# Kernel optimization log

Measured on AMD Instinct MI355X. Metric: run time of the kernel, lower is better.

## Reference

```python
import jax, jax.numpy as jnp
import numpy as np

N_NODES = 50000
N_EDGES = 600000
IN_FEATS = 128
OUT_FEATS = 128


def setup_inputs() -> dict:
    key = jax.random.key(0)
    k1, k2, k3, k4, k5 = jax.random.split(key, 5)
    feature = jax.random.normal(k1, (N_NODES, IN_FEATS), dtype=jnp.float32)
    src = jax.random.randint(k2, (N_EDGES,), 0, N_NODES, dtype=jnp.int64)
    dst = jax.random.randint(k3, (N_EDGES,), 0, N_NODES, dtype=jnp.int64)
    # nn.Linear params (PyTorch stores weight as [out, in])
    bound = 1.0 / np.sqrt(IN_FEATS)
    W = jax.random.uniform(k4, (OUT_FEATS, IN_FEATS), dtype=jnp.float32, minval=-bound, maxval=bound)
    b = jax.random.uniform(k5, (OUT_FEATS,), dtype=jnp.float32, minval=-bound, maxval=bound)
    return {"feature": feature, "W": W, "b": b, "src": src, "dst": dst}


def reference(feature, W, b, src, dst):
    # copy_src + sum: aggregate src features onto dst nodes (SpMM)
    agg = jax.ops.segment_sum(feature[src], dst, num_segments=N_NODES)  # [N, in]
    # linear + tanh
    return jnp.tanh(agg @ W.T + b)  # [N, out]
```

## Files before the change

kernel.cpp:

```cpp
#include <hip/hip_runtime.h>
#include <hip/hip_fp16.h>
#include <math.h>

constexpr int kNodes = 50000;
constexpr int kEdges = 600000;
constexpr int kF     = 128;
constexpr int kNPB   = 64;
constexpr int kCap   = 48;

constexpr int kGemmB = (kNodes + kNPB - 1) / kNPB;
constexpr int kFillB = (kEdges + 255) / 256;

constexpr size_t kOffWt     = 0;
constexpr size_t kOffCursor = 65536;
constexpr size_t kOffBucket = 65536 + 200192;
constexpr size_t kOffGpk    = kOffBucket + (size_t)kNodes * kCap * 4;
constexpr size_t kWsNeeded  = kOffGpk + (size_t)kNodes * kF * 2;

static __device__ __forceinline__ unsigned int packh2(float a, float b) {
    __half2 h = __floats2half2_rn(a, b);
    return *reinterpret_cast<unsigned int*>(&h);
}

__global__ __launch_bounds__(256) void prep0(const float* __restrict__ W,
                                             float* __restrict__ Wt,
                                             int* __restrict__ cursor) {
    int gid = blockIdx.x * 256 + threadIdx.x;
    if (gid < kF * kF) {
        int k = gid >> 7;
        int o = gid & (kF - 1);
        Wt[gid] = W[o * kF + k];
    }
    if (gid < kNodes) cursor[gid] = 0;
}

__global__ __launch_bounds__(256, 4) void gemm_fill(const float* __restrict__ F,
                                                    const float* __restrict__ Wt,
                                                    const int* __restrict__ src,
                                                    const int* __restrict__ dst,
                                                    int* __restrict__ cursor,
                                                    int* __restrict__ bucket,
                                                    uint2* __restrict__ Gpk2) {
    __shared__ float sF[kNPB * kF];

    const int t = threadIdx.x;

    if (blockIdx.x >= kGemmB) {
        int e = (blockIdx.x - kGemmB) * 256 + t;
        if (e < kEdges) {
            int d = dst[e];
            int p = atomicAdd(&cursor[d], 1);
            if (p < kCap) bucket[d * kCap + p] = src[e];
        }
        return;
    }

    const int n0 = blockIdx.x * kNPB;
    const int rows = min(kNPB, kNodes - n0);
    for (int i = t * 4; i < rows * kF; i += 256 * 4) {
        *reinterpret_cast<float4*>(&sF[i]) =
            *reinterpret_cast<const float4*>(F + (size_t)n0 * kF + i);
    }
    __syncthreads();

    const int tn = t >> 5;
    const int to = t & 31;
    const int nb = tn * 8;

    float acc[8][4];
#pragma unroll
    for (int n = 0; n < 8; ++n)
#pragma unroll
        for (int j = 0; j < 4; ++j) acc[n][j] = 0.0f;

    for (int k = 0; k < kF; k += 4) {
        float4 wt[4];
#pragma unroll
        for (int i = 0; i < 4; ++i)
            wt[i] = *reinterpret_cast<const float4*>(Wt + (k + i) * kF + to * 4);
#pragma unroll
        for (int n = 0; n < 8; ++n) {
            float4 av = *reinterpret_cast<const float4*>(&sF[(nb + n) * kF + k]);
#pragma unroll
            for (int j = 0; j < 4; ++j) {
                const float* wj0 = reinterpret_cast<const float*>(&wt[0]);
                const float* wj1 = reinterpret_cast<const float*>(&wt[1]);
                const float* wj2 = reinterpret_cast<const float*>(&wt[2]);
                const float* wj3 = reinterpret_cast<const float*>(&wt[3]);
                acc[n][j] += av.x * wj0[j];
                acc[n][j] += av.y * wj1[j];
                acc[n][j] += av.z * wj2[j];
                acc[n][j] += av.w * wj3[j];
            }
        }
    }

#pragma unroll
    for (int n = 0; n < 8; ++n) {
        int node = n0 + nb + n;
        if (node < kNodes) {
            uint2 p;
            p.x = packh2(acc[n][0], acc[n][1]);
            p.y = packh2(acc[n][2], acc[n][3]);
            Gpk2[(size_t)node * 32 + to] = p;
        }
    }
}

__global__ __launch_bounds__(256) void gather_tanh(const uint4* __restrict__ Gpk4,
                                                   const int* __restrict__ bucket,
                                                   const int* __restrict__ cursor,
                                                   const float* __restrict__ bias,
                                                   float* __restrict__ out) {
    const int wave = (blockIdx.x * 256 + threadIdx.x) >> 6;
    const int lane = threadIdx.x & 63;
    if (wave >= kNodes) return;
    const int grp = lane >> 4;
    const int sub = lane & 15;

    const int deg = min(cursor[wave], kCap);
    const int base = wave * kCap;

    int eid = (lane < deg) ? bucket[base + lane] : 0;

    float acc[8];
#pragma unroll
    for (int i = 0; i < 8; ++i) acc[i] = 0.0f;

    const int iters = (deg + 3) >> 2;
#pragma unroll 2
    for (int i = 0; i < iters; ++i) {
        const int j = grp + 4 * i;
        const bool valid = (j < deg);
        int s = __shfl(eid, valid ? j : 0);
        if (valid) {
            uint4 u = Gpk4[(size_t)s * 16 + sub];
            const __half2* hp = reinterpret_cast<const __half2*>(&u);
#pragma unroll
            for (int q = 0; q < 4; ++q) {
                float2 f = __half22float2(hp[q]);
                acc[2 * q]     += f.x;
                acc[2 * q + 1] += f.y;
            }
        }
    }

#pragma unroll
    for (int i = 0; i < 8; ++i) {
        acc[i] += __shfl_xor(acc[i], 16);
        acc[i] += __shfl_xor(acc[i], 32);
    }

    if (grp == 0) {
        float4 b0 = *reinterpret_cast<const float4*>(bias + sub * 8);
        float4 b1 = *reinterpret_cast<const float4*>(bias + sub * 8 + 4);
        float4 r0, r1;
        r0.x = 1.0f - 2.0f / (__expf(2.0f * (acc[0] + b0.x)) + 1.0f);
        r0.y = 1.0f - 2.0f / (__expf(2.0f * (acc[1] + b0.y)) + 1.0f);
        r0.z = 1.0f - 2.0f / (__expf(2.0f * (acc[2] + b0.z)) + 1.0f);
        r0.w = 1.0f - 2.0f / (__expf(2.0f * (acc[3] + b0.w)) + 1.0f);
        r1.x = 1.0f - 2.0f / (__expf(2.0f * (acc[4] + b1.x)) + 1.0f);
        r1.y = 1.0f - 2.0f / (__expf(2.0f * (acc[5] + b1.y)) + 1.0f);
        r1.z = 1.0f - 2.0f / (__expf(2.0f * (acc[6] + b1.z)) + 1.0f);
        r1.w = 1.0f - 2.0f / (__expf(2.0f * (acc[7] + b1.w)) + 1.0f);
        float4* dst = reinterpret_cast<float4*>(out + (size_t)wave * kF + sub * 8);
        dst[0] = r0;
        dst[1] = r1;
    }
}

__global__ __launch_bounds__(256) void scatter_add(const float* __restrict__ feature,
                                                   const int* __restrict__ src,
                                                   const int* __restrict__ dst,
                                                   float* __restrict__ agg) {
    int gid = blockIdx.x * 256 + threadIdx.x;
    int e = gid >> 5;
    int c = (gid & 31) << 2;
    float4 v = *reinterpret_cast<const float4*>(feature + (size_t)src[e] * kF + c);
    float* p = agg + (size_t)dst[e] * kF + c;
    atomicAdd(p + 0, v.x);
    atomicAdd(p + 1, v.y);
    atomicAdd(p + 2, v.z);
    atomicAdd(p + 3, v.w);
}

__global__ __launch_bounds__(256, 4) void linear_tanh(float* __restrict__ inout,
                                                      const float* __restrict__ Wt,
                                                      const float* __restrict__ bias) {
    __shared__ float sAgg[kNPB * kF];
    __shared__ float sB[kF];
    const int t  = threadIdx.x;
    const int n0 = blockIdx.x * kNPB;
    if (t < kF) sB[t] = bias[t];
    const int rows = min(kNPB, kNodes - n0);
    for (int i = t * 4; i < rows * kF; i += 256 * 4)
        *reinterpret_cast<float4*>(&sAgg[i]) =
            *reinterpret_cast<const float4*>(inout + (size_t)n0 * kF + i);
    __syncthreads();
    const int tn = t >> 5, to = t & 31, nb = tn * 8;
    float acc[8][4];
#pragma unroll
    for (int n = 0; n < 8; ++n)
#pragma unroll
        for (int j = 0; j < 4; ++j) acc[n][j] = 0.0f;
    for (int k = 0; k < kF; k += 4) {
        float4 wt[4];
#pragma unroll
        for (int i = 0; i < 4; ++i)
            wt[i] = *reinterpret_cast<const float4*>(Wt + (k + i) * kF + to * 4);
#pragma unroll
        for (int n = 0; n < 8; ++n) {
            float4 av = *reinterpret_cast<const float4*>(&sAgg[(nb + n) * kF + k]);
#pragma unroll
            for (int j = 0; j < 4; ++j) {
                const float* w0 = reinterpret_cast<const float*>(&wt[0]);
                const float* w1 = reinterpret_cast<const float*>(&wt[1]);
                const float* w2 = reinterpret_cast<const float*>(&wt[2]);
                const float* w3 = reinterpret_cast<const float*>(&wt[3]);
                acc[n][j] += av.x * w0[j] + av.y * w1[j] + av.z * w2[j] + av.w * w3[j];
            }
        }
    }
#pragma unroll
    for (int n = 0; n < 8; ++n) {
        int node = n0 + nb + n;
        if (node < kNodes) {
            float4 r;
            r.x = 1.0f - 2.0f / (__expf(2.0f * (acc[n][0] + sB[to * 4 + 0])) + 1.0f);
            r.y = 1.0f - 2.0f / (__expf(2.0f * (acc[n][1] + sB[to * 4 + 1])) + 1.0f);
            r.z = 1.0f - 2.0f / (__expf(2.0f * (acc[n][2] + sB[to * 4 + 2])) + 1.0f);
            r.w = 1.0f - 2.0f / (__expf(2.0f * (acc[n][3] + sB[to * 4 + 3])) + 1.0f);
            *reinterpret_cast<float4*>(inout + (size_t)node * kF + to * 4) = r;
        }
    }
}

extern "C" void kernel_launch(void* const* d_in, const int* in_sizes, int n_in,
                              void* d_out, int out_size, void* d_ws, size_t ws_size,
                              hipStream_t stream) {
    const float* feature = (const float*)d_in[0];
    const float* W       = (const float*)d_in[1];
    const float* b       = (const float*)d_in[2];
    const int*   src     = (const int*)d_in[3];
    const int*   dst     = (const int*)d_in[4];
    float* out = (float*)d_out;

    char* ws = (char*)d_ws;
    float* Wt     = (float*)(ws + kOffWt);
    int*   cursor = (int*)(ws + kOffCursor);
    int*   bucket = (int*)(ws + kOffBucket);
    uint2* Gpk2   = (uint2*)(ws + kOffGpk);

    if (ws_size >= kWsNeeded) {
        prep0<<<(kNodes + 255) / 256, 256, 0, stream>>>(W, Wt, cursor);
        gemm_fill<<<kGemmB + kFillB, 256, 0, stream>>>(
            feature, Wt, src, dst, cursor, bucket, Gpk2);
        gather_tanh<<<(kNodes + 3) / 4, 256, 0, stream>>>(
            (const uint4*)Gpk2, bucket, cursor, b, out);
    } else {
        prep0<<<(kNodes + 255) / 256, 256, 0, stream>>>(W, Wt, cursor);
        hipMemsetAsync(out, 0, (size_t)kNodes * kF * sizeof(float), stream);
        scatter_add<<<(kEdges * 32) / 256, 256, 0, stream>>>(feature, src, dst, out);
        linear_tanh<<<(kNodes + kNPB - 1) / kNPB, 256, 0, stream>>>(out, Wt, b);
    }
}
```

Before: 145.9 us.

## Use fp16 packed dot products in transform GEMM with LDS-staged weights

The per-node linear transform now converts features and W to half precision in shared memory and accumulates with packed fp16 dot2 instructions into fp32. Each thread now handles output columns strided by 32, so the gather kernel reads a permuted bias and writes outputs with strided float2 stores. The goal is to cut ALU and LDS traffic in the GEMM phase. In exchange, every block repacks the full weight matrix, LDS use grows so occupancy bound drops to 3, and rounding inputs to fp16 reduces accuracy.

Result: slower. 163.6 us (+12.2%).

```diff
diff --git a/kernel.cpp b/kernel.cpp
--- a/kernel.cpp
+++ b/kernel.cpp
@@ -15,7 +15,20 @@
 constexpr size_t kOffCursor = 65536;
 constexpr size_t kOffBucket = 65536 + 200192;
 constexpr size_t kOffGpk    = kOffBucket + (size_t)kNodes * kCap * 4;
-constexpr size_t kWsNeeded  = kOffGpk + (size_t)kNodes * kF * 2;
+constexpr size_t kOffBiasP  = kOffGpk + (size_t)kNodes * kF * 2;
+constexpr size_t kWsNeeded  = kOffBiasP + kF * 4;
+
+typedef _Float16 v2h __attribute__((ext_vector_type(2)));
+union H8 { uint4 u; v2h h[4]; };
+
+#if __has_builtin(__builtin_amdgcn_fdot2)
+#define FDOT2(a, b, c) __builtin_amdgcn_fdot2((a), (b), (c), false)
+#else
+static __device__ __forceinline__ float fdot2_emul(v2h a, v2h b, float c) {
+    return c + (float)a[0] * (float)b[0] + (float)a[1] * (float)b[1];
+}
+#define FDOT2(a, b, c) fdot2_emul((a), (b), (c))
+#endif
 
 static __device__ __forceinline__ unsigned int packh2(float a, float b) {
     __half2 h = __floats2half2_rn(a, b);
@@ -23,25 +36,29 @@
 }
 
 __global__ __launch_bounds__(256) void prep0(const float* __restrict__ W,
+                                             const float* __restrict__ b,
                                              float* __restrict__ Wt,
-                                             int* __restrict__ cursor) {
+                                             int* __restrict__ cursor,
+                                             float* __restrict__ bias_p) {
     int gid = blockIdx.x * 256 + threadIdx.x;
     if (gid < kF * kF) {
         int k = gid >> 7;
         int o = gid & (kF - 1);
         Wt[gid] = W[o * kF + k];
     }
+    if (gid < kF) bias_p[gid] = b[(gid >> 2) + 32 * (gid & 3)];
     if (gid < kNodes) cursor[gid] = 0;
 }
 
-__global__ __launch_bounds__(256, 4) void gemm_fill(const float* __restrict__ F,
-                                                    const float* __restrict__ Wt,
+__global__ __launch_bounds__(256, 3) void gemm_fill(const float* __restrict__ F,
+                                                    const float* __restrict__ Wg,
                                                     const int* __restrict__ src,
                                                     const int* __restrict__ dst,
                                                     int* __restrict__ cursor,
                                                     int* __restrict__ bucket,
                                                     uint2* __restrict__ Gpk2) {
-    __shared__ float sF[kNPB * kF];
+    __shared__ unsigned short sW[kF * kF];
+    __shared__ unsigned short sF[kNPB * kF];
 
     const int t = threadIdx.x;
 
@@ -57,9 +74,25 @@
 
     const int n0 = blockIdx.x * kNPB;
     const int rows = min(kNPB, kNodes - n0);
+
+    for (int idx = t; idx < kF * 16; idx += 256) {
+        int o  = idx >> 4;
+        int K8 = idx & 15;
+        const float4* wp = reinterpret_cast<const float4*>(Wg + o * kF + K8 * 8);
+        float4 w0 = wp[0], w1 = wp[1];
+        uint4 pk;
+        pk.x = packh2(w0.x, w0.y);
+        pk.y = packh2(w0.z, w0.w);
+        pk.z = packh2(w1.x, w1.y);
+        pk.w = packh2(w1.z, w1.w);
+        *reinterpret_cast<uint4*>(&sW[(K8 * kF + o) * 8]) = pk;
+    }
     for (int i = t * 4; i < rows * kF; i += 256 * 4) {
-        *reinterpret_cast<float4*>(&sF[i]) =
-            *reinterpret_cast<const float4*>(F + (size_t)n0 * kF + i);
+        float4 v = *reinterpret_cast<const float4*>(F + (size_t)n0 * kF + i);
+        uint2 pk;
+        pk.x = packh2(v.x, v.y);
+        pk.y = packh2(v.z, v.w);
+        *reinterpret_cast<uint2*>(&sF[i]) = pk;
     }
     __syncthreads();
 
@@ -73,24 +106,21 @@
 #pragma unroll
         for (int j = 0; j < 4; ++j) acc[n][j] = 0.0f;
 
-    for (int k = 0; k < kF; k += 4) {
-        float4 wt[4];
-#pragma unroll
-        for (int i = 0; i < 4; ++i)
-            wt[i] = *reinterpret_cast<const float4*>(Wt + (k + i) * kF + to * 4);
+#pragma unroll 4
+    for (int K8 = 0; K8 < 16; ++K8) {
+        H8 w[4];
+#pragma unroll
+        for (int j = 0; j < 4; ++j)
+            w[j].u = *reinterpret_cast<const uint4*>(&sW[(K8 * kF + to + 32 * j) * 8]);
 #pragma unroll
         for (int n = 0; n < 8; ++n) {
-            float4 av = *reinterpret_cast<const float4*>(&sF[(nb + n) * kF + k]);
+            H8 a;
+            a.u = *reinterpret_cast<const uint4*>(&sF[(nb + n) * kF + K8 * 8]);
 #pragma unroll
             for (int j = 0; j < 4; ++j) {
-                const float* wj0 = reinterpret_cast<const float*>(&wt[0]);
-                const float* wj1 = reinterpret_cast<const float*>(&wt[1]);
-                const float* wj2 = reinterpret_cast<const float*>(&wt[2]);
-                const float* wj3 = reinterpret_cast<const float*>(&wt[3]);
-                acc[n][j] += av.x * wj0[j];
-                acc[n][j] += av.y * wj1[j];
-                acc[n][j] += av.z * wj2[j];
-                acc[n][j] += av.w * wj3[j];
+#pragma unroll
+                for (int p = 0; p < 4; ++p)
+                    acc[n][j] = FDOT2(a.h[p], w[j].h[p], acc[n][j]);
             }
         }
     }
@@ -110,7 +140,7 @@
 __global__ __launch_bounds__(256) void gather_tanh(const uint4* __restrict__ Gpk4,
                                                    const int* __restrict__ bucket,
                                                    const int* __restrict__ cursor,
-                                                   const float* __restrict__ bias,
+                                                   const float* __restrict__ bias_p,
                                                    float* __restrict__ out) {
     const int wave = (blockIdx.x * 256 + threadIdx.x) >> 6;
     const int lane = threadIdx.x & 63;
@@ -152,20 +182,21 @@
     }
 
     if (grp == 0) {
-        float4 b0 = *reinterpret_cast<const float4*>(bias + sub * 8);
-        float4 b1 = *reinterpret_cast<const float4*>(bias + sub * 8 + 4);
-        float4 r0, r1;
-        r0.x = 1.0f - 2.0f / (__expf(2.0f * (acc[0] + b0.x)) + 1.0f);
-        r0.y = 1.0f - 2.0f / (__expf(2.0f * (acc[1] + b0.y)) + 1.0f);
-        r0.z = 1.0f - 2.0f / (__expf(2.0f * (acc[2] + b0.z)) + 1.0f);
-        r0.w = 1.0f - 2.0f / (__expf(2.0f * (acc[3] + b0.w)) + 1.0f);
-        r1.x = 1.0f - 2.0f / (__expf(2.0f * (acc[4] + b1.x)) + 1.0f);
-        r1.y = 1.0f - 2.0f / (__expf(2.0f * (acc[5] + b1.y)) + 1.0f);
-        r1.z = 1.0f - 2.0f / (__expf(2.0f * (acc[6] + b1.z)) + 1.0f);
-        r1.w = 1.0f - 2.0f / (__expf(2.0f * (acc[7] + b1.w)) + 1.0f);
-        float4* dst = reinterpret_cast<float4*>(out + (size_t)wave * kF + sub * 8);
-        dst[0] = r0;
-        dst[1] = r1;
+        float4 b0 = *reinterpret_cast<const float4*>(bias_p + sub * 8);
+        float4 b1 = *reinterpret_cast<const float4*>(bias_p + sub * 8 + 4);
+        float r[8];
+        r[0] = 1.0f - 2.0f / (__expf(2.0f * (acc[0] + b0.x)) + 1.0f);
+        r[1] = 1.0f - 2.0f / (__expf(2.0f * (acc[1] + b0.y)) + 1.0f);
+        r[2] = 1.0f - 2.0f / (__expf(2.0f * (acc[2] + b0.z)) + 1.0f);
+        r[3] = 1.0f - 2.0f / (__expf(2.0f * (acc[3] + b0.w)) + 1.0f);
+        r[4] = 1.0f - 2.0f / (__expf(2.0f * (acc[4] + b1.x)) + 1.0f);
+        r[5] = 1.0f - 2.0f / (__expf(2.0f * (acc[5] + b1.y)) + 1.0f);
+        r[6] = 1.0f - 2.0f / (__expf(2.0f * (acc[6] + b1.z)) + 1.0f);
+        r[7] = 1.0f - 2.0f / (__expf(2.0f * (acc[7] + b1.w)) + 1.0f);
+        float* op = out + (size_t)wave * kF + 2 * sub;
+#pragma unroll
+        for (int q = 0; q < 4; ++q)
+            *reinterpret_cast<float2*>(op + 32 * q) = make_float2(r[q], r[q + 4]);
     }
 }
 
@@ -250,15 +281,16 @@
     int*   cursor = (int*)(ws + kOffCursor);
     int*   bucket = (int*)(ws + kOffBucket);
     uint2* Gpk2   = (uint2*)(ws + kOffGpk);
+    float* bias_p = (float*)(ws + kOffBiasP);
 
     if (ws_size >= kWsNeeded) {
-        prep0<<<(kNodes + 255) / 256, 256, 0, stream>>>(W, Wt, cursor);
+        prep0<<<(kNodes + 255) / 256, 256, 0, stream>>>(W, b, Wt, cursor, bias_p);
         gemm_fill<<<kGemmB + kFillB, 256, 0, stream>>>(
-            feature, Wt, src, dst, cursor, bucket, Gpk2);
+            feature, W, src, dst, cursor, bucket, Gpk2);
         gather_tanh<<<(kNodes + 3) / 4, 256, 0, stream>>>(
-            (const uint4*)Gpk2, bucket, cursor, b, out);
+            (const uint4*)Gpk2, bucket, cursor, bias_p, out);
     } else {
-        prep0<<<(kNodes + 255) / 256, 256, 0, stream>>>(W, Wt, cursor);
+        prep0<<<(kNodes + 255) / 256, 256, 0, stream>>>(W, b, Wt, cursor, bias_p);
         hipMemsetAsync(out, 0, (size_t)kNodes * kF * sizeof(float), stream);
         scatter_add<<<(kEdges * 32) / 256, 256, 0, stream>>>(feature, src, dst, out);
         linear_tanh<<<(kNodes + kNPB - 1) / kNPB, 256, 0, stream>>>(out, Wt, b);
```

## Compute node-feature GEMM with fp16 MFMA instead of fp32 FMA

Applied to the files above, without the earlier changes.

The GEMM part of gemm_fill now converts the weight matrix and a 64-row feature tile to fp16 in padded shared memory. It then uses 16x16x32 fp16 MFMA instructions, with each wave handling 16 nodes across all 128 outputs. This replaces the scalar fp32 FMA loop and is meant to cut compute time in the fused GEMM/fill kernel. In exchange it adds fp16 rounding of inputs, more shared memory (which lowers the occupancy hint to 3), and each block reconverting the full W.

Result: slower. 161.2 us (+10.5%).

```diff
diff --git a/kernel.cpp b/kernel.cpp
--- a/kernel.cpp
+++ b/kernel.cpp
@@ -7,6 +7,7 @@
 constexpr int kF     = 128;
 constexpr int kNPB   = 64;
 constexpr int kCap   = 48;
+constexpr int kStr   = 136;
 
 constexpr int kGemmB = (kNodes + kNPB - 1) / kNPB;
 constexpr int kFillB = (kEdges + 255) / 256;
@@ -16,6 +17,9 @@
 constexpr size_t kOffBucket = 65536 + 200192;
 constexpr size_t kOffGpk    = kOffBucket + (size_t)kNodes * kCap * 4;
 constexpr size_t kWsNeeded  = kOffGpk + (size_t)kNodes * kF * 2;
+
+typedef _Float16 v8h __attribute__((ext_vector_type(8)));
+typedef float    v4f __attribute__((ext_vector_type(4)));
 
 static __device__ __forceinline__ unsigned int packh2(float a, float b) {
     __half2 h = __floats2half2_rn(a, b);
@@ -34,14 +38,15 @@
     if (gid < kNodes) cursor[gid] = 0;
 }
 
-__global__ __launch_bounds__(256, 4) void gemm_fill(const float* __restrict__ F,
-                                                    const float* __restrict__ Wt,
+__global__ __launch_bounds__(256, 3) void gemm_fill(const float* __restrict__ F,
+                                                    const float* __restrict__ Wg,
                                                     const int* __restrict__ src,
                                                     const int* __restrict__ dst,
                                                     int* __restrict__ cursor,
                                                     int* __restrict__ bucket,
                                                     uint2* __restrict__ Gpk2) {
-    __shared__ float sF[kNPB * kF];
+    __shared__ __align__(16) unsigned short sW[kF * kStr];
+    __shared__ __align__(16) unsigned short sF[kNPB * kStr];
 
     const int t = threadIdx.x;
 
@@ -57,52 +62,55 @@
 
     const int n0 = blockIdx.x * kNPB;
     const int rows = min(kNPB, kNodes - n0);
-    for (int i = t * 4; i < rows * kF; i += 256 * 4) {
-        *reinterpret_cast<float4*>(&sF[i]) =
-            *reinterpret_cast<const float4*>(F + (size_t)n0 * kF + i);
+
+    for (int idx = t; idx < kF * 16; idx += 256) {
+        int o = idx >> 4, c = idx & 15;
+        const float4* wp = reinterpret_cast<const float4*>(Wg + o * kF + c * 8);
+        float4 w0 = wp[0], w1 = wp[1];
+        uint4 pk;
+        pk.x = packh2(w0.x, w0.y);
+        pk.y = packh2(w0.z, w0.w);
+        pk.z = packh2(w1.x, w1.y);
+        pk.w = packh2(w1.z, w1.w);
+        *reinterpret_cast<uint4*>(&sW[o * kStr + c * 8]) = pk;
+    }
+    for (int idx = t; idx < rows * 16; idx += 256) {
+        int n = idx >> 4, c = idx & 15;
+        const float4* fp = reinterpret_cast<const float4*>(F + (size_t)(n0 + n) * kF + c * 8);
+        float4 f0 = fp[0], f1 = fp[1];
+        uint4 pk;
+        pk.x = packh2(f0.x, f0.y);
+        pk.y = packh2(f0.z, f0.w);
+        pk.z = packh2(f1.x, f1.y);
+        pk.w = packh2(f1.z, f1.w);
+        *reinterpret_cast<uint4*>(&sF[n * kStr + c * 8]) = pk;
     }
     __syncthreads();
 
-    const int tn = t >> 5;
-    const int to = t & 31;
-    const int nb = tn * 8;
-
-    float acc[8][4];
-#pragma unroll
-    for (int n = 0; n < 8; ++n)
-#pragma unroll
-        for (int j = 0; j < 4; ++j) acc[n][j] = 0.0f;
-
-    for (int k = 0; k < kF; k += 4) {
-        float4 wt[4];
-#pragma unroll
-        for (int i = 0; i < 4; ++i)
-            wt[i] = *reinterpret_cast<const float4*>(Wt + (k + i) * kF + to * 4);
-#pragma unroll
-        for (int n = 0; n < 8; ++n) {
-            float4 av = *reinterpret_cast<const float4*>(&sF[(nb + n) * kF + k]);
-#pragma unroll
-            for (int j = 0; j < 4; ++j) {
-                const float* wj0 = reinterpret_cast<const float*>(&wt[0]);
-                const float* wj1 = reinterpret_cast<const float*>(&wt[1]);
-                const float* wj2 = reinterpret_cast<const float*>(&wt[2]);
-                const float* wj3 = reinterpret_cast<const float*>(&wt[3]);
-                acc[n][j] += av.x * wj0[j];
-                acc[n][j] += av.y * wj1[j];
-                acc[n][j] += av.z * wj2[j];
-                acc[n][j] += av.w * wj3[j];
-            }
-        }
-    }
-
-#pragma unroll
-    for (int n = 0; n < 8; ++n) {
-        int node = n0 + nb + n;
+    const int wv   = t >> 6;
+    const int lane = t & 63;
+    const int m    = lane & 15;
+    const int quad = lane >> 4;
+
+    v8h bfrag[4];
+#pragma unroll
+    for (int kc = 0; kc < 4; ++kc)
+        bfrag[kc] = *reinterpret_cast<const v8h*>(&sF[(wv * 16 + m) * kStr + kc * 32 + quad * 8]);
+
+    const int node = n0 + wv * 16 + m;
+#pragma unroll
+    for (int ot = 0; ot < 8; ++ot) {
+        v4f acc = {0.0f, 0.0f, 0.0f, 0.0f};
+#pragma unroll
+        for (int kc = 0; kc < 4; ++kc) {
+            v8h afrag = *reinterpret_cast<const v8h*>(&sW[(ot * 16 + m) * kStr + kc * 32 + quad * 8]);
+            acc = __builtin_amdgcn_mfma_f32_16x16x32_f16(afrag, bfrag[kc], acc, 0, 0, 0);
+        }
         if (node < kNodes) {
             uint2 p;
-            p.x = packh2(acc[n][0], acc[n][1]);
-            p.y = packh2(acc[n][2], acc[n][3]);
-            Gpk2[(size_t)node * 32 + to] = p;
+            p.x = packh2(acc[0], acc[1]);
+            p.y = packh2(acc[2], acc[3]);
+            Gpk2[(size_t)node * 32 + ot * 4 + quad] = p;
         }
     }
 }
@@ -254,7 +262,7 @@
     if (ws_size >= kWsNeeded) {
         prep0<<<(kNodes + 255) / 256, 256, 0, stream>>>(W, Wt, cursor);
         gemm_fill<<<kGemmB + kFillB, 256, 0, stream>>>(
-            feature, Wt, src, dst, cursor, bucket, Gpk2);
+            feature, W, src, dst, cursor, bucket, Gpk2);
         gather_tanh<<<(kNodes + 3) / 4, 256, 0, stream>>>(
             (const uint4*)Gpk2, bucket, cursor, b, out);
     } else {
```
